# Kernel optimization log

Hardware: AMD Instinct MI355X
Metric: run time of the kernel (lower is better)

Reference implementation:

```python
import jax, jax.numpy as jnp
import numpy as np

B, S, D = 2, 1024, 4096
H, KVH = 32, 8
HD = D // H          # 128
N_REP = H // KVH     # 4
R = 2                # LoRA rank


def setup_inputs() -> dict:
    key = jax.random.key(0)
    ks = jax.random.split(key, 10)
    sc = 0.02
    x = jax.random.normal(ks[0], (B, S, D), jnp.float32)
    wq = jax.random.normal(ks[1], (D, H * HD), jnp.float32) * sc
    wk = jax.random.normal(ks[2], (D, KVH * HD), jnp.float32) * sc
    wv = jax.random.normal(ks[3], (D, KVH * HD), jnp.float32) * sc
    wo = jax.random.normal(ks[4], (H * HD, D), jnp.float32) * sc
    lora_q_a = jax.random.normal(ks[5], (D, R), jnp.float32) * sc
    lora_q_b = jax.random.normal(ks[6], (R, H * HD), jnp.float32) * sc
    lora_v_a = jax.random.normal(ks[7], (D, R), jnp.float32) * sc
    lora_v_b = jax.random.normal(ks[8], (R, KVH * HD), jnp.float32) * sc
    # RoPE frequencies: freqs_cis[t, i] = exp(1j * t * 10000^(-2i/HD))
    inv_freq = 1.0 / (10000.0 ** (jnp.arange(0, HD, 2, dtype=jnp.float32) / HD))  # [HD/2]
    t = jnp.arange(S, dtype=jnp.float32)
    ang = jnp.outer(t, inv_freq)                      # [S, HD/2]
    freqs_cos = jnp.cos(ang)
    freqs_sin = jnp.sin(ang)
    # causal additive mask [1, 1, S, S]
    mask = jnp.triu(jnp.full((S, S), -1e9, jnp.float32), k=1)[None, None]
    return {"x": x, "wq": wq, "wk": wk, "wv": wv, "wo": wo,
            "lora_q_a": lora_q_a, "lora_q_b": lora_q_b,
            "lora_v_a": lora_v_a, "lora_v_b": lora_v_b,
            "freqs_cos": freqs_cos, "freqs_sin": freqs_sin,
            "mask": mask, "start_pos": 0}


def _rope(t, cos, sin):
    # t: [B, S, h, HD]; pairs (even, odd) are (real, imag) of complex halves
    b, s, h, hd = t.shape
    tr = t.reshape(b, s, h, hd // 2, 2)
    a, bb = tr[..., 0], tr[..., 1]
    c = cos[None, :, None, :]
    sn = sin[None, :, None, :]
    out = jnp.stack([a * c - bb * sn, a * sn + bb * c], axis=-1)
    return out.reshape(b, s, h, hd)


def reference(x, wq, wk, wv, wo, lora_q_a, lora_q_b, lora_v_a, lora_v_b,
              freqs_cos, freqs_sin, mask, start_pos):
    # projections + LoRA (note: original Lora_layer applies NO scaling in forward)
    xq = x @ wq + (x @ lora_q_a) @ lora_q_b            # [B,S,H*HD]
    xk = x @ wk                                         # [B,S,KVH*HD]
    xv = x @ wv + (x @ lora_v_a) @ lora_v_b             # [B,S,KVH*HD]
    xq = xq.reshape(B, S, H, HD)
    xk = xk.reshape(B, S, KVH, HD)
    xv = xv.reshape(B, S, KVH, HD)
    xq = _rope(xq, freqs_cos, freqs_sin)
    xk = _rope(xk, freqs_cos, freqs_sin)
    # repeat_kv (GQA expansion): [B,S,KVH,HD] -> [B,S,H,HD]
    k = jnp.repeat(xk, N_REP, axis=2)
    v = jnp.repeat(xv, N_REP, axis=2)
    # attention
    scores = jnp.einsum('bshd,bthd->bhst', xq, k) / np.sqrt(HD).astype(np.float32)
    scores = scores + mask
    probs = jax.nn.softmax(scores.astype(jnp.float32), axis=-1).astype(xq.dtype)
    out = jnp.einsum('bhst,bthd->bshd', probs, v)       # [B,S,H,HD]
    out = out.reshape(B, S, H * HD) @ wo                # [B,S,D]
    return out
```

## Files before the change

kernel.cpp:

```cpp
#include <hip/hip_runtime.h>
#include <stdint.h>

#define B_ 2
#define S_ 1024
#define D_ 4096
#define H_ 32
#define KVH_ 8
#define HD_ 128

typedef short short8 __attribute__((ext_vector_type(8)));
typedef float floatx4 __attribute__((ext_vector_type(4)));

__device__ __forceinline__ ushort f2bf(float f) {
  union { float f; uint32_t u; } v; v.f = f;
  return (ushort)((v.u + 0x7FFFu + ((v.u >> 16) & 1u)) >> 16);
}

__device__ __forceinline__ void gload16(const void* g, void* l) {
  __builtin_amdgcn_global_load_lds((__attribute__((address_space(1))) void*)g,
                                   (__attribute__((address_space(3))) void*)l,
                                   16, 0, 0);
}

__global__ __launch_bounds__(256) void k_cvtlora(const float* __restrict__ x,
                                                 const float* __restrict__ qa,
                                                 const float* __restrict__ va,
                                                 ushort* __restrict__ xb,
                                                 float* __restrict__ xa) {
  const int row = blockIdx.x, t = threadIdx.x;
  const float* xr = x + (size_t)row * D_;
  ushort* xo = xb + (size_t)row * D_;
  float a0 = 0, a1 = 0, a2 = 0, a3 = 0;
#pragma unroll
  for (int it = 0; it < 4; it++) {
    const int i = it * 1024 + t * 4;
    float4 v = *(const float4*)(xr + i);
    ushort o4[4] = {f2bf(v.x), f2bf(v.y), f2bf(v.z), f2bf(v.w)};
    *(uint2*)(xo + i) = *(uint2*)o4;
    float4 q0 = *(const float4*)(qa + 2 * i);
    float4 q1 = *(const float4*)(qa + 2 * i + 4);
    float4 w0 = *(const float4*)(va + 2 * i);
    float4 w1 = *(const float4*)(va + 2 * i + 4);
    a0 += v.x * q0.x + v.y * q0.z + v.z * q1.x + v.w * q1.z;
    a1 += v.x * q0.y + v.y * q0.w + v.z * q1.y + v.w * q1.w;
    a2 += v.x * w0.x + v.y * w0.z + v.z * w1.x + v.w * w1.z;
    a3 += v.x * w0.y + v.y * w0.w + v.z * w1.y + v.w * w1.w;
  }
#pragma unroll
  for (int off = 32; off; off >>= 1) {
    a0 += __shfl_down(a0, off, 64);
    a1 += __shfl_down(a1, off, 64);
    a2 += __shfl_down(a2, off, 64);
    a3 += __shfl_down(a3, off, 64);
  }
  __shared__ float red[4][4];
  const int w = t >> 6, lane = t & 63;
  if (lane == 0) { red[w][0] = a0; red[w][1] = a1; red[w][2] = a2; red[w][3] = a3; }
  __syncthreads();
  if (t < 4)
    xa[(size_t)row * 4 + t] = red[0][t] + red[1][t] + red[2][t] + red[3][t];
}

__global__ __launch_bounds__(256) void k_tr4(const float* __restrict__ in,
                                             ushort* __restrict__ out,
                                             int in_stride, int out_stride) {
  __shared__ float t[64][65];
  const int n0 = blockIdx.x * 64, k0 = blockIdx.y * 64;
  const int c4 = (threadIdx.x & 15) * 4, r = threadIdx.x >> 4;
#pragma unroll
  for (int rr = 0; rr < 64; rr += 16) {
    float4 v = *(const float4*)&in[(size_t)(k0 + r + rr) * in_stride + n0 + c4];
    t[r + rr][c4] = v.x; t[r + rr][c4 + 1] = v.y;
    t[r + rr][c4 + 2] = v.z; t[r + rr][c4 + 3] = v.w;
  }
  __syncthreads();
#pragma unroll
  for (int rr = 0; rr < 64; rr += 16) {
    const int n = r + rr;
    ushort o4[4] = {f2bf(t[c4][n]), f2bf(t[c4 + 1][n]),
                    f2bf(t[c4 + 2][n]), f2bf(t[c4 + 3][n])};
    *(uint2*)&out[(size_t)(n0 + n) * out_stride + k0 + c4] = *(uint2*)o4;
  }
}

__global__ __launch_bounds__(256) void k_add(const float* __restrict__ a,
                                             const float* __restrict__ b,
                                             float* __restrict__ o, int n4) {
  int i = blockIdx.x * 256 + threadIdx.x;
  if (i >= n4) return;
  float4 x = ((const float4*)a)[i], y = ((const float4*)b)[i];
  float4 r = {x.x + y.x, x.y + y.y, x.z + y.z, x.w + y.w};
  ((float4*)o)[i] = r;
}

#define GBAR __builtin_amdgcn_s_barrier()
#define LGKM0 asm volatile("s_waitcnt lgkmcnt(0)" ::: "memory")
#define LGKM8 asm volatile("s_waitcnt lgkmcnt(8)" ::: "memory")
#define VMCNT0 asm volatile("s_waitcnt vmcnt(0)" ::: "memory")

#define QSTAGE_A(KT) do {                                                    \
    const ushort* gp_ = A + (size_t)(m0 + w * 16 + srow) * Kz + (KT) * 64 + scol; \
    char* lp_ = qlds + ((KT) & 1) * 65536 + w * 2048;                        \
    gload16(gp_, lp_);  gload16(gp_ + 8 * Kz, lp_ + 1024);                   \
  } while (0)

#define QSTAGE_B(U, KT) do {                                                 \
    const ushort* gp_ = Bt + (size_t)(n0 + (U) * 128 + w * 16 + srow) * Kz   \
                          + (KT) * 64 + scol;                                \
    char* lp_ = qlds + ((KT) & 1) * 65536 + 16384 + (U) * 16384 + w * 2048;  \
    gload16(gp_, lp_);  gload16(gp_ + 8 * Kz, lp_ + 1024);                   \
  } while (0)

#define QLOAD_AF(BUF) do {                                                   \
    const char* ab_ = qlds + (BUF) * 65536 + (wr * 64 + lr) * 128;           \
    _Pragma("unroll") for (int fr = 0; fr < 4; fr++)                         \
    _Pragma("unroll") for (int ks = 0; ks < 2; ks++)                         \
      af[fr][ks] = *(const short8*)(ab_ + fr * 2048 + (((ks * 4 + g) * 16) ^ swz)); \
  } while (0)

#define QLOAD_BF(J, BUF) do {                                                \
    const char* bb_ = qlds + (BUF) * 65536 + 16384 + (J) * 16384 + (wc * 32 + lr) * 128; \
    _Pragma("unroll") for (int e = 0; e < 2; e++)                            \
    _Pragma("unroll") for (int ks = 0; ks < 2; ks++)                         \
      bf[e][ks] = *(const short8*)(bb_ + e * 2048 + (((ks * 4 + g) * 16) ^ swz)); \
  } while (0)

#define QMFMA(J) do {                                                        \
    __builtin_amdgcn_s_setprio(1);                                           \
    _Pragma("unroll") for (int fr = 0; fr < 4; fr++)                         \
    _Pragma("unroll") for (int e = 0; e < 2; e++)                            \
    _Pragma("unroll") for (int ks = 0; ks < 2; ks++)                         \
      acc[fr][(J) * 2 + e] = __builtin_amdgcn_mfma_f32_16x16x32_bf16(        \
          af[fr][ks], bf[e][ks], acc[fr][(J) * 2 + e], 0, 0, 0);             \
    __builtin_amdgcn_s_setprio(0);                                           \
  } while (0)

__global__ __launch_bounds__(512, 2) void k_gemmq(const ushort* __restrict__ A,
                                                  const ushort* __restrict__ Bt,
                                                  float* __restrict__ C,
                                                  const float* __restrict__ xa,
                                                  const float* __restrict__ qb,
                                                  const float* __restrict__ vb) {
  __shared__ char qlds[131072];
  const int flat = blockIdx.y * 16 + blockIdx.x;
  const int swz_id = (flat & 7) * 32 + (flat >> 3);
  const int m0 = (swz_id >> 4) * 128, n0 = (swz_id & 15) * 384;
  const int tid = threadIdx.x, lane = tid & 63, w = tid >> 6;
  const int wr = w >> 2, wc = w & 3;
  const int lr = lane & 15, g = lane >> 4;
  const int swz = (lr & 7) * 16;
  const size_t Kz = 4096;
  const int NK = 64;
  const int srow = lane >> 3;
  const int scol = ((lane & 7) ^ (srow & 7)) * 8;

  floatx4 acc[4][6] = {};
  short8 af[4][2], bf[2][2];

  QSTAGE_A(0); QSTAGE_B(0, 0); QSTAGE_B(1, 0); QSTAGE_B(2, 0);
  QSTAGE_A(1); QSTAGE_B(0, 1); QSTAGE_B(1, 1);
  asm volatile("s_waitcnt vmcnt(10)" ::: "memory");
  GBAR;

  for (int t = 0; t < NK; ++t) {
    const int c = t & 1;
    QLOAD_AF(c); QLOAD_BF(0, c);
    if (t + 1 < NK) QSTAGE_B(2, t + 1);
    LGKM8;
    GBAR; LGKM0; QMFMA(0);
    if (t >= NK - 1) { VMCNT0; }
    else { asm volatile("s_waitcnt vmcnt(10)" ::: "memory"); }
    GBAR;
    QLOAD_BF(1, c);
    if (t + 2 < NK) { QSTAGE_A(t + 2); QSTAGE_B(0, t + 2); }
    GBAR; LGKM0; QMFMA(1);
    if (t >= NK - 2) { VMCNT0; }
    else { asm volatile("s_waitcnt vmcnt(12)" ::: "memory"); }
    GBAR;
    QLOAD_BF(2, c);
    if (t + 2 < NK) QSTAGE_B(1, t + 2);
    GBAR; LGKM0; QMFMA(2);
    if (t >= NK - 2) { VMCNT0; }
    else { asm volatile("s_waitcnt vmcnt(10)" ::: "memory"); }
    GBAR;
  }

#pragma unroll
  for (int fr = 0; fr < 4; fr++) {
    const int mb = m0 + wr * 64 + fr * 16 + g * 4;
    float4 xa4[4];
#pragma unroll
    for (int r = 0; r < 4; r++) xa4[r] = *(const float4*)&xa[(size_t)(mb + r) * 4];
#pragma unroll
    for (int j = 0; j < 3; j++)
#pragma unroll
      for (int e = 0; e < 2; e++) {
        const int n = n0 + j * 128 + wc * 32 + e * 16 + lr;
        const bool lq = (n < 4096), lv = (n >= 5120);
        float b0 = 0.f, b1 = 0.f;
        if (lq) { b0 = qb[n]; b1 = qb[4096 + n]; }
        else if (lv) { b0 = vb[n - 5120]; b1 = vb[1024 + n - 5120]; }
#pragma unroll
        for (int r = 0; r < 4; r++) {
          float cc = acc[fr][j * 2 + e][r];
          if (lq)      cc += xa4[r].x * b0 + xa4[r].y * b1;
          else if (lv) cc += xa4[r].z * b0 + xa4[r].w * b1;
          C[(size_t)(mb + r) * 6144 + n] = cc;
        }
      }
  }
}

#define STAGE_A(HALF, KT) do {                                               \
    const ushort* gp_ = A + (size_t)(m0 + (HALF) * 128 + w * 16 + srow) * Kz \
                          + kz0 + (KT) * 64 + scol;                          \
    char* lp_ = lds + ((KT) & 1) * 65536 + (HALF) * 16384 + w * 2048;        \
    gload16(gp_, lp_);                                                       \
    gload16(gp_ + 8 * Kz, lp_ + 1024);                                       \
  } while (0)

#define STAGE_B(HALF, KT) do {                                               \
    const ushort* gp_ = Bt + (size_t)(n0 + (HALF) * 128 + w * 16 + srow) * Kz\
                          + kz0 + (KT) * 64 + scol;                          \
    char* lp_ = lds + ((KT) & 1) * 65536 + 32768 + (HALF) * 16384 + w * 2048;\
    gload16(gp_, lp_);                                                       \
    gload16(gp_ + 8 * Kz, lp_ + 1024);                                       \
  } while (0)

#define LOAD_AF(QA, BUF) do {                                                \
    const char* ab_ = lds + (BUF) * 65536 + (QA) * 16384 + (wr * 64 + lr) * 128; \
    _Pragma("unroll") for (int fr = 0; fr < 4; fr++)                         \
    _Pragma("unroll") for (int ks = 0; ks < 2; ks++)                         \
      af[fr][ks] = *(const short8*)(ab_ + fr * 2048 + (((ks * 4 + g) * 16) ^ swz)); \
  } while (0)

#define LOAD_BF(QB, BUF, BF) do {                                            \
    const char* bb_ = lds + (BUF) * 65536 + 32768 + (QB) * 16384 + (wc * 32 + lr) * 128; \
    _Pragma("unroll") for (int fc = 0; fc < 2; fc++)                         \
    _Pragma("unroll") for (int ks = 0; ks < 2; ks++)                         \
      BF[fc][ks] = *(const short8*)(bb_ + fc * 2048 + (((ks * 4 + g) * 16) ^ swz)); \
  } while (0)

#define MFMA16(QA, QB, BF) do {                                              \
    __builtin_amdgcn_s_setprio(1);                                           \
    _Pragma("unroll") for (int fr = 0; fr < 4; fr++)                         \
    _Pragma("unroll") for (int fc = 0; fc < 2; fc++)                         \
    _Pragma("unroll") for (int ks = 0; ks < 2; ks++)                         \
      acc[(QA) * 4 + fr][(QB) * 2 + fc] = __builtin_amdgcn_mfma_f32_16x16x32_bf16( \
          af[fr][ks], BF[fc][ks], acc[(QA) * 4 + fr][(QB) * 2 + fc], 0, 0, 0);     \
    __builtin_amdgcn_s_setprio(0);                                           \
  } while (0)

#define VMCNT6 asm volatile("s_waitcnt vmcnt(6)" ::: "memory")

__global__ __launch_bounds__(512, 2) void k_gemm8(const ushort* __restrict__ A,
                                                  const ushort* __restrict__ Bt,
                                                  float* __restrict__ C0,
                                                  float* __restrict__ C1,
                                                  int N, int K) {
  __shared__ char lds[131072];
  const int nbx = gridDim.x;
  const int nwg = nbx * gridDim.y;
  const int flat = blockIdx.y * nbx + blockIdx.x;
  const int swz_id = (flat & 7) * (nwg >> 3) + (flat >> 3);
  const int m0 = (swz_id / nbx) * 256, n0 = (swz_id % nbx) * 256;
  const int kspan = K / gridDim.z;
  const int kz0 = blockIdx.z * kspan;
  const int NK = kspan >> 6;
  const int NJ = NK >> 1;
  float* __restrict__ Cout = blockIdx.z ? C1 : C0;

  const int tid = threadIdx.x, lane = tid & 63, w = tid >> 6;
  const int wr = w >> 2, wc = w & 3;
  const int lr = lane & 15, g = lane >> 4;
  const int swz = (lr & 7) * 16;
  const size_t Kz = (size_t)K;
  const int srow = lane >> 3;
  const int scol = ((lane & 7) ^ (srow & 7)) * 8;

  floatx4 acc[8][4] = {};
  short8 af[4][2], bf0[2][2], bf1[2][2];

  STAGE_A(0, 0); STAGE_B(0, 0); STAGE_A(1, 0); STAGE_B(1, 0);
  STAGE_A(0, 1); STAGE_B(0, 1); STAGE_A(1, 1);
  VMCNT6;
  GBAR;

  for (int j = 0; j < NJ; ++j) {
    const int t0 = 2 * j, t1 = 2 * j + 1;
    const bool last = (j == NJ - 1);
    LOAD_AF(0, 0);
    LOAD_BF(0, 0, bf0);
    STAGE_B(1, t1);
    GBAR; LGKM0; MFMA16(0, 0, bf0); GBAR;
    LOAD_BF(1, 0, bf1);
    if (t0 + 2 < NK) STAGE_A(0, t0 + 2);
    GBAR; LGKM0; MFMA16(0, 1, bf1); GBAR;
    LOAD_AF(1, 0);
    if (t0 + 2 < NK) STAGE_B(0, t0 + 2);
    GBAR; LGKM0; MFMA16(1, 1, bf1); GBAR;
    if (t0 + 2 < NK) STAGE_A(1, t0 + 2);
    if (last) { VMCNT0; } else { VMCNT6; }
    GBAR; LGKM0; MFMA16(1, 0, bf0); GBAR;
    LOAD_AF(0, 1);
    LOAD_BF(0, 1, bf0);
    if (t0 + 2 < NK) STAGE_B(1, t0 + 2);
    GBAR; LGKM0; MFMA16(0, 0, bf0); GBAR;
    LOAD_BF(1, 1, bf1);
    if (t1 + 2 < NK) STAGE_A(0, t1 + 2);
    GBAR; LGKM0; MFMA16(0, 1, bf1); GBAR;
    LOAD_AF(1, 1);
    if (t1 + 2 < NK) STAGE_B(0, t1 + 2);
    GBAR; LGKM0; MFMA16(1, 1, bf1); GBAR;
    if (t1 + 2 < NK) STAGE_A(1, t1 + 2);
    if (last) { VMCNT0; } else { VMCNT6; }
    GBAR; LGKM0; MFMA16(1, 0, bf0); GBAR;
  }

#pragma unroll
  for (int qa = 0; qa < 2; qa++)
#pragma unroll
    for (int fr = 0; fr < 4; fr++) {
      const int mb = m0 + qa * 128 + wr * 64 + fr * 16 + g * 4;
#pragma unroll
      for (int qb_ = 0; qb_ < 2; qb_++)
#pragma unroll
        for (int fc = 0; fc < 2; fc++) {
          const int n = n0 + qb_ * 128 + wc * 32 + fc * 16 + lr;
#pragma unroll
          for (int r = 0; r < 4; r++)
            Cout[(size_t)(mb + r) * N + n] = acc[qa * 4 + fr][qb_ * 2 + fc][r];
        }
    }
}

__global__ __launch_bounds__(256) void k_rope(const float* __restrict__ xqkv,
                                              const float* __restrict__ fcos,
                                              const float* __restrict__ fsin,
                                              ushort* __restrict__ Qb,
                                              ushort* __restrict__ Kb) {
  const int s = blockIdx.x, b = blockIdx.y;
  const float* row = xqkv + (size_t)(b * S_ + s) * 6144;
#pragma unroll
  for (int it = 0; it < 8; it++) {
    int p2 = it * 256 + threadIdx.x;
    int h = p2 >> 6, p = p2 & 63;
    float2 ab = *(const float2*)(row + h * 128 + 2 * p);
    float c = fcos[s * 64 + p], sn = fsin[s * 64 + p];
    uint32_t pk = (uint32_t)f2bf(ab.x * c - ab.y * sn) |
                  ((uint32_t)f2bf(ab.x * sn + ab.y * c) << 16);
    *(uint32_t*)(Qb + ((size_t)(b * H_ + h) * S_ + s) * HD_ + 2 * p) = pk;
  }
#pragma unroll
  for (int it = 0; it < 2; it++) {
    int p2 = it * 256 + threadIdx.x;
    int h = p2 >> 6, p = p2 & 63;
    float2 ab = *(const float2*)(row + 4096 + h * 128 + 2 * p);
    float c = fcos[s * 64 + p], sn = fsin[s * 64 + p];
    uint32_t pk = (uint32_t)f2bf(ab.x * c - ab.y * sn) |
                  ((uint32_t)f2bf(ab.x * sn + ab.y * c) << 16);
    *(uint32_t*)(Kb + ((size_t)(b * KVH_ + h) * S_ + s) * HD_ + 2 * p) = pk;
  }
}

#define FSTAGE(T, DB) do {                                                   \
    _Pragma("unroll") for (int i_ = 0; i_ < 4; i_++) {                       \
      gload16(Kg + (size_t)((T) * 64 + i_ * 16 + k_srow) * HD_ + k_scol,     \
              fls + (DB) * 16384 + i_ * 4096 + w * 1024);                    \
      gload16(Vg + (size_t)(i_ * 32 + v_srow) * S_ + (T) * 64 + v_scol,      \
              fls + 32768 + (DB) * 16384 + i_ * 4096 + w * 1024);            \
    }                                                                        \
  } while (0)

__global__ __launch_bounds__(256, 2) void k_flash(const ushort* __restrict__ Qb,
                                                  const ushort* __restrict__ Kb,
                                                  const ushort* __restrict__ Vt,
                                                  ushort* __restrict__ attn) {
  __shared__ char fls[73728];
  const int qblk = (gridDim.x - 1) - blockIdx.x;
  const int h = blockIdx.y, b = blockIdx.z;
  const int kvh = h >> 2;
  const int tid = threadIdx.x, w = tid >> 6, lane = tid & 63;
  const int lr = lane & 15, g = lane >> 4;
  const int swz = (lr & 7) * 16;
  const int qr0 = qblk * 64 + w * 16;
  const ushort* Qrow = Qb + ((size_t)(b * H_ + h) * S_ + qr0 + lr) * HD_;
  short8 qf[4];
#pragma unroll
  for (int ks = 0; ks < 4; ks++) qf[ks] = *(const short8*)(Qrow + ks * 32 + g * 8);
  const ushort* Kg = Kb + (size_t)(b * KVH_ + kvh) * S_ * HD_;
  const ushort* Vg = Vt + (size_t)(b * KVH_ + kvh) * HD_ * S_;
  char* Pw = fls + 65536 + w * 2048;
  const int q7 = lr & 7;
  const int k_srow = tid >> 4;
  const int k_scol = ((tid & 15) ^ (k_srow & 7)) * 8;
  const int v_srow = tid >> 3;
  const int v_scol = ((tid & 7) ^ (v_srow & 7)) * 8;

  float m_run = -1e30f, l_run = 0.f;
  floatx4 o[8] = {};
  const int nt = qblk + 1;

  FSTAGE(0, 0);
  asm volatile("s_waitcnt vmcnt(0)" ::: "memory");
  __builtin_amdgcn_s_barrier();

  for (int t = 0; t < nt; t++) {
    const int cur = t & 1;
    if (t + 1 < nt) FSTAGE(t + 1, cur ^ 1);
    const char* Kl = fls + cur * 16384;
    const char* Vl = fls + 32768 + cur * 16384;
    floatx4 s4[4] = {};
    __builtin_amdgcn_s_setprio(1);
#pragma unroll
    for (int mf = 0; mf < 4; mf++) {
      const char* Krow = Kl + (mf * 16 + lr) * 256;
#pragma unroll
      for (int ks = 0; ks < 4; ks++) {
        short8 kf = *(const short8*)(Krow + (((ks * 4 + g) * 16) ^ swz));
        s4[mf] = __builtin_amdgcn_mfma_f32_16x16x32_bf16(kf, qf[ks], s4[mf], 0, 0, 0);
      }
    }
    __builtin_amdgcn_s_setprio(0);
    const float scale = 0.088388347648318447f;
    float tm = -1e30f;
    if (t == nt - 1) {
#pragma unroll
      for (int mf = 0; mf < 4; mf++)
#pragma unroll
        for (int r = 0; r < 4; r++) {
          int kv = t * 64 + mf * 16 + g * 4 + r;
          float v = (kv > qr0 + lr) ? -1e30f : s4[mf][r] * scale;
          s4[mf][r] = v;
          tm = fmaxf(tm, v);
        }
    } else {
#pragma unroll
      for (int mf = 0; mf < 4; mf++)
#pragma unroll
        for (int r = 0; r < 4; r++) {
          float v = s4[mf][r] * scale;
          s4[mf][r] = v;
          tm = fmaxf(tm, v);
        }
    }
    tm = fmaxf(tm, __shfl_xor(tm, 16, 64));
    tm = fmaxf(tm, __shfl_xor(tm, 32, 64));
    float m_new = fmaxf(m_run, tm);
    float corr = __expf(m_run - m_new);
    float rs = 0.f;
#pragma unroll
    for (int mf = 0; mf < 4; mf++)
#pragma unroll
      for (int r = 0; r < 4; r++) {
        float p = __expf(s4[mf][r] - m_new);
        s4[mf][r] = p;
        rs += p;
      }
    rs += __shfl_xor(rs, 16, 64);
    rs += __shfl_xor(rs, 32, 64);
    l_run = l_run * corr + rs;
    m_run = m_new;
#pragma unroll
    for (int r = 0; r < 4; r++) {
      float cr = __shfl(corr, g * 4 + r, 64);
#pragma unroll
      for (int nf = 0; nf < 8; nf++) o[nf][r] *= cr;
    }
#pragma unroll
    for (int mf = 0; mf < 4; mf++) {
      uint2 pv;
      pv.x = (uint32_t)f2bf(s4[mf][0]) | ((uint32_t)f2bf(s4[mf][1]) << 16);
      pv.y = (uint32_t)f2bf(s4[mf][2]) | ((uint32_t)f2bf(s4[mf][3]) << 16);
      *(uint2*)(Pw + lr * 128 + ((mf * 32 + g * 8) ^ (q7 << 4))) = pv;
    }
    __builtin_amdgcn_s_setprio(1);
#pragma unroll
    for (int ks2 = 0; ks2 < 2; ks2++) {
      short8 pa = *(const short8*)(Pw + lr * 128 + ((ks2 * 64 + g * 16) ^ (q7 << 4)));
#pragma unroll
      for (int nf = 0; nf < 8; nf++) {
        short8 vf = *(const short8*)(Vl + (nf * 16 + lr) * 128 + (((ks2 * 4 + g) * 16) ^ swz));
        o[nf] = __builtin_amdgcn_mfma_f32_16x16x32_bf16(pa, vf, o[nf], 0, 0, 0);
      }
    }
    __builtin_amdgcn_s_setprio(0);
    asm volatile("s_waitcnt vmcnt(0)" ::: "memory");
    __builtin_amdgcn_s_barrier();
  }
  float linv = 1.0f / l_run;
  ushort* outp = attn + ((size_t)(b * S_) + qr0) * 4096 + h * 128;
#pragma unroll
  for (int r = 0; r < 4; r++) {
    float li = __shfl(linv, g * 4 + r, 64);
    ushort* orow = outp + (size_t)(g * 4 + r) * 4096;
#pragma unroll
    for (int nf = 0; nf < 8; nf++)
      orow[nf * 16 + lr] = f2bf(o[nf][r] * li);
  }
}

extern "C" void kernel_launch(void* const* d_in, const int* in_sizes, int n_in,
                              void* d_out, int out_size, void* d_ws, size_t ws_size,
                              hipStream_t stream) {
  (void)in_sizes; (void)n_in; (void)out_size; (void)ws_size;
  const float* x    = (const float*)d_in[0];
  const float* wq   = (const float*)d_in[1];
  const float* wk   = (const float*)d_in[2];
  const float* wv   = (const float*)d_in[3];
  const float* wo   = (const float*)d_in[4];
  const float* lqa  = (const float*)d_in[5];
  const float* lqb  = (const float*)d_in[6];
  const float* lva  = (const float*)d_in[7];
  const float* lvb  = (const float*)d_in[8];
  const float* fcos = (const float*)d_in[9];
  const float* fsin = (const float*)d_in[10];

  char* ws = (char*)d_ws;
  ushort* xb   = (ushort*)(ws + 0);
  ushort* wT   = (ushort*)(ws + 16777216);
  ushort* woT  = (ushort*)(ws + 67108864);
  float*  xqkv = (float*) (ws + 100663296);
  ushort* Qb   = (ushort*)(ws + 150994944);
  ushort* Kb   = (ushort*)(ws + 167772160);
  ushort* Vt   = (ushort*)(ws + 171966464);
  ushort* attn = (ushort*)(ws + 176160768);
  float*  xa   = (float*) (ws + 192937984);
  float*  p0   = (float*) (ws + 16777216);
  float*  p1   = (float*) (ws + 100663296);

  k_cvtlora<<<2048, 256, 0, stream>>>(x, lqa, lva, xb, xa);
  k_tr4<<<dim3(64, 64), 256, 0, stream>>>(wq, wT, 4096, 4096);
  k_tr4<<<dim3(16, 64), 256, 0, stream>>>(wk, wT + (size_t)4096 * 4096, 1024, 4096);
  k_tr4<<<dim3(16, 64), 256, 0, stream>>>(wv, wT + (size_t)5120 * 4096, 1024, 4096);
  k_tr4<<<dim3(64, 64), 256, 0, stream>>>(wo, woT, 4096, 4096);
  k_gemmq<<<dim3(16, 16), 512, 0, stream>>>(xb, wT, xqkv, xa, lqb, lvb);
  k_rope<<<dim3(1024, 2), 256, 0, stream>>>(xqkv, fcos, fsin, Qb, Kb);
  k_tr4<<<dim3(16, 16), 256, 0, stream>>>(xqkv + 5120, Vt, 6144, 1024);
  k_tr4<<<dim3(16, 16), 256, 0, stream>>>(xqkv + (size_t)1024 * 6144 + 5120, Vt + 1048576, 6144, 1024);
  k_flash<<<dim3(16, 32, 2), 256, 0, stream>>>(Qb, Kb, Vt, attn);
  k_gemm8<<<dim3(16, 8, 2), 512, 0, stream>>>(attn, woT, p0, p1, 4096, 4096);
  k_add<<<8192, 256, 0, stream>>>(p0, p1, (float*)d_out, 2097152);
}
```

Baseline: 335.1 us.

## Fuse launches, emit bf16 QKV with transposed V, widen flash tiles, drop split-K

Merges the weight-transpose launches into two z-indexed kernels. The QKV GEMM now writes bf16 Q/K and transposed V directly, which removes the fp32 intermediate and the separate V transpose kernels. The flash kernel processes 128 query rows per block with two accumulators that share K/V tiles, halving K/V traffic per query. The output projection replaces split-K plus an add kernel with a single 128x256-tile GEMM writing the output directly. The trade-offs are fewer blocks in flash and the output GEMM, lower occupancy potential, and bf16 rounding of the projections before RoPE.

```diff
diff --git a/kernel.cpp b/kernel.cpp
--- a/kernel.cpp
+++ b/kernel.cpp
@@ -14,6 +14,9 @@
 __device__ __forceinline__ ushort f2bf(float f) {
   union { float f; uint32_t u; } v; v.f = f;
   return (ushort)((v.u + 0x7FFFu + ((v.u >> 16) & 1u)) >> 16);
+}
+__device__ __forceinline__ float bf2f(ushort u) {
+  union { uint32_t x; float f; } v; v.x = ((uint32_t)u) << 16; return v.f;
 }
 
 __device__ __forceinline__ void gload16(const void* g, void* l) {
@@ -61,9 +64,13 @@
     xa[(size_t)row * 4 + t] = red[0][t] + red[1][t] + red[2][t] + red[3][t];
 }
 
-__global__ __launch_bounds__(256) void k_tr4(const float* __restrict__ in,
-                                             ushort* __restrict__ out,
-                                             int in_stride, int out_stride) {
+__global__ __launch_bounds__(256) void k_trw2(const float* __restrict__ in0,
+                                              const float* __restrict__ in1,
+                                              ushort* __restrict__ out0,
+                                              ushort* __restrict__ out1,
+                                              int in_stride, int out_stride) {
+  const float* in = blockIdx.z ? in1 : in0;
+  ushort* out = blockIdx.z ? out1 : out0;
   __shared__ float t[64][65];
   const int n0 = blockIdx.x * 64, k0 = blockIdx.y * 64;
   const int c4 = (threadIdx.x & 15) * 4, r = threadIdx.x >> 4;
@@ -83,20 +90,12 @@
   }
 }
 
-__global__ __launch_bounds__(256) void k_add(const float* __restrict__ a,
-                                             const float* __restrict__ b,
-                                             float* __restrict__ o, int n4) {
-  int i = blockIdx.x * 256 + threadIdx.x;
-  if (i >= n4) return;
-  float4 x = ((const float4*)a)[i], y = ((const float4*)b)[i];
-  float4 r = {x.x + y.x, x.y + y.y, x.z + y.z, x.w + y.w};
-  ((float4*)o)[i] = r;
-}
-
 #define GBAR __builtin_amdgcn_s_barrier()
 #define LGKM0 asm volatile("s_waitcnt lgkmcnt(0)" ::: "memory")
 #define LGKM8 asm volatile("s_waitcnt lgkmcnt(8)" ::: "memory")
 #define VMCNT0 asm volatile("s_waitcnt vmcnt(0)" ::: "memory")
+#define VMCNT2 asm volatile("s_waitcnt vmcnt(2)" ::: "memory")
+#define VMCNT6 asm volatile("s_waitcnt vmcnt(6)" ::: "memory")
 
 #define QSTAGE_A(KT) do {                                                    \
     const ushort* gp_ = A + (size_t)(m0 + w * 16 + srow) * Kz + (KT) * 64 + scol; \
@@ -137,7 +136,8 @@
 
 __global__ __launch_bounds__(512, 2) void k_gemmq(const ushort* __restrict__ A,
                                                   const ushort* __restrict__ Bt,
-                                                  float* __restrict__ C,
+                                                  ushort* __restrict__ xq,
+                                                  ushort* __restrict__ Vt,
                                                   const float* __restrict__ xa,
                                                   const float* __restrict__ qb,
                                                   const float* __restrict__ vb) {
@@ -188,6 +188,7 @@
 #pragma unroll
   for (int fr = 0; fr < 4; fr++) {
     const int mb = m0 + wr * 64 + fr * 16 + g * 4;
+    const int bb = mb >> 10, s0 = mb & 1023;
     float4 xa4[4];
 #pragma unroll
     for (int r = 0; r < 4; r++) xa4[r] = *(const float4*)&xa[(size_t)(mb + r) * 4];
@@ -196,169 +197,149 @@
 #pragma unroll
       for (int e = 0; e < 2; e++) {
         const int n = n0 + j * 128 + wc * 32 + e * 16 + lr;
-        const bool lq = (n < 4096), lv = (n >= 5120);
-        float b0 = 0.f, b1 = 0.f;
-        if (lq) { b0 = qb[n]; b1 = qb[4096 + n]; }
-        else if (lv) { b0 = vb[n - 5120]; b1 = vb[1024 + n - 5120]; }
-#pragma unroll
-        for (int r = 0; r < 4; r++) {
-          float cc = acc[fr][j * 2 + e][r];
-          if (lq)      cc += xa4[r].x * b0 + xa4[r].y * b1;
-          else if (lv) cc += xa4[r].z * b0 + xa4[r].w * b1;
-          C[(size_t)(mb + r) * 6144 + n] = cc;
+        if (n < 5120) {
+          const bool lq = (n < 4096);
+          float b0 = 0.f, b1 = 0.f;
+          if (lq) { b0 = qb[n]; b1 = qb[4096 + n]; }
+#pragma unroll
+          for (int r = 0; r < 4; r++) {
+            float cc = acc[fr][j * 2 + e][r];
+            if (lq) cc += xa4[r].x * b0 + xa4[r].y * b1;
+            xq[(size_t)(mb + r) * 6144 + n] = f2bf(cc);
+          }
+        } else {
+          const int vcol = n - 5120;
+          const float b0 = vb[vcol], b1 = vb[1024 + vcol];
+          ushort v4[4];
+#pragma unroll
+          for (int r = 0; r < 4; r++)
+            v4[r] = f2bf(acc[fr][j * 2 + e][r] + xa4[r].z * b0 + xa4[r].w * b1);
+          *(uint2*)&Vt[(size_t)((bb * 8 + (vcol >> 7)) * 128 + (vcol & 127)) * 1024 + s0] =
+              *(uint2*)v4;
         }
       }
   }
 }
 
-#define STAGE_A(HALF, KT) do {                                               \
-    const ushort* gp_ = A + (size_t)(m0 + (HALF) * 128 + w * 16 + srow) * Kz \
-                          + kz0 + (KT) * 64 + scol;                          \
-    char* lp_ = lds + ((KT) & 1) * 65536 + (HALF) * 16384 + w * 2048;        \
-    gload16(gp_, lp_);                                                       \
-    gload16(gp_ + 8 * Kz, lp_ + 1024);                                       \
-  } while (0)
-
-#define STAGE_B(HALF, KT) do {                                               \
-    const ushort* gp_ = Bt + (size_t)(n0 + (HALF) * 128 + w * 16 + srow) * Kz\
-                          + kz0 + (KT) * 64 + scol;                          \
-    char* lp_ = lds + ((KT) & 1) * 65536 + 32768 + (HALF) * 16384 + w * 2048;\
-    gload16(gp_, lp_);                                                       \
-    gload16(gp_ + 8 * Kz, lp_ + 1024);                                       \
-  } while (0)
-
-#define LOAD_AF(QA, BUF) do {                                                \
-    const char* ab_ = lds + (BUF) * 65536 + (QA) * 16384 + (wr * 64 + lr) * 128; \
+#define OSTAGE_A(KT) do {                                                    \
+    const ushort* gp_ = A + (size_t)(m0 + w * 16 + srow) * Kz + (KT) * 64 + scol; \
+    char* lp_ = olds + ((KT) & 1) * 49152 + w * 2048;                        \
+    gload16(gp_, lp_);  gload16(gp_ + 8 * Kz, lp_ + 1024);                   \
+  } while (0)
+
+#define OSTAGE_B(U, KT) do {                                                 \
+    const ushort* gp_ = Bt + (size_t)(n0 + (U) * 128 + w * 16 + srow) * Kz   \
+                          + (KT) * 64 + scol;                                \
+    char* lp_ = olds + ((KT) & 1) * 49152 + 16384 + (U) * 16384 + w * 2048;  \
+    gload16(gp_, lp_);  gload16(gp_ + 8 * Kz, lp_ + 1024);                   \
+  } while (0)
+
+#define OLOAD_AF(BUF) do {                                                   \
+    const char* ab_ = olds + (BUF) * 49152 + (wr * 64 + lr) * 128;           \
     _Pragma("unroll") for (int fr = 0; fr < 4; fr++)                         \
     _Pragma("unroll") for (int ks = 0; ks < 2; ks++)                         \
       af[fr][ks] = *(const short8*)(ab_ + fr * 2048 + (((ks * 4 + g) * 16) ^ swz)); \
   } while (0)
 
-#define LOAD_BF(QB, BUF, BF) do {                                            \
-    const char* bb_ = lds + (BUF) * 65536 + 32768 + (QB) * 16384 + (wc * 32 + lr) * 128; \
-    _Pragma("unroll") for (int fc = 0; fc < 2; fc++)                         \
+#define OLOAD_BF(U, BUF) do {                                                \
+    const char* bb_ = olds + (BUF) * 49152 + 16384 + (U) * 16384 + (wc * 32 + lr) * 128; \
+    _Pragma("unroll") for (int e = 0; e < 2; e++)                            \
     _Pragma("unroll") for (int ks = 0; ks < 2; ks++)                         \
-      BF[fc][ks] = *(const short8*)(bb_ + fc * 2048 + (((ks * 4 + g) * 16) ^ swz)); \
-  } while (0)
-
-#define MFMA16(QA, QB, BF) do {                                              \
+      bf[e][ks] = *(const short8*)(bb_ + e * 2048 + (((ks * 4 + g) * 16) ^ swz)); \
+  } while (0)
+
+#define OMFMA(U) do {                                                        \
     __builtin_amdgcn_s_setprio(1);                                           \
     _Pragma("unroll") for (int fr = 0; fr < 4; fr++)                         \
-    _Pragma("unroll") for (int fc = 0; fc < 2; fc++)                         \
+    _Pragma("unroll") for (int e = 0; e < 2; e++)                            \
     _Pragma("unroll") for (int ks = 0; ks < 2; ks++)                         \
-      acc[(QA) * 4 + fr][(QB) * 2 + fc] = __builtin_amdgcn_mfma_f32_16x16x32_bf16( \
-          af[fr][ks], BF[fc][ks], acc[(QA) * 4 + fr][(QB) * 2 + fc], 0, 0, 0);     \
+      acc[fr][(U) * 2 + e] = __builtin_amdgcn_mfma_f32_16x16x32_bf16(        \
+          af[fr][ks], bf[e][ks], acc[fr][(U) * 2 + e], 0, 0, 0);             \
     __builtin_amdgcn_s_setprio(0);                                           \
   } while (0)
 
-#define VMCNT6 asm volatile("s_waitcnt vmcnt(6)" ::: "memory")
-
-__global__ __launch_bounds__(512, 2) void k_gemm8(const ushort* __restrict__ A,
+__global__ __launch_bounds__(512, 2) void k_gemmo(const ushort* __restrict__ A,
                                                   const ushort* __restrict__ Bt,
-                                                  float* __restrict__ C0,
-                                                  float* __restrict__ C1,
-                                                  int N, int K) {
-  __shared__ char lds[131072];
-  const int nbx = gridDim.x;
-  const int nwg = nbx * gridDim.y;
-  const int flat = blockIdx.y * nbx + blockIdx.x;
-  const int swz_id = (flat & 7) * (nwg >> 3) + (flat >> 3);
-  const int m0 = (swz_id / nbx) * 256, n0 = (swz_id % nbx) * 256;
-  const int kspan = K / gridDim.z;
-  const int kz0 = blockIdx.z * kspan;
-  const int NK = kspan >> 6;
-  const int NJ = NK >> 1;
-  float* __restrict__ Cout = blockIdx.z ? C1 : C0;
-
+                                                  float* __restrict__ C) {
+  __shared__ char olds[98304];
+  const int flat = blockIdx.y * 16 + blockIdx.x;
+  const int swz_id = (flat & 7) * 32 + (flat >> 3);
+  const int m0 = (swz_id >> 4) * 128, n0 = (swz_id & 15) * 256;
   const int tid = threadIdx.x, lane = tid & 63, w = tid >> 6;
   const int wr = w >> 2, wc = w & 3;
   const int lr = lane & 15, g = lane >> 4;
   const int swz = (lr & 7) * 16;
-  const size_t Kz = (size_t)K;
+  const size_t Kz = 4096;
+  const int NK = 64;
   const int srow = lane >> 3;
   const int scol = ((lane & 7) ^ (srow & 7)) * 8;
 
-  floatx4 acc[8][4] = {};
-  short8 af[4][2], bf0[2][2], bf1[2][2];
-
-  STAGE_A(0, 0); STAGE_B(0, 0); STAGE_A(1, 0); STAGE_B(1, 0);
-  STAGE_A(0, 1); STAGE_B(0, 1); STAGE_A(1, 1);
-  VMCNT6;
+  floatx4 acc[4][4] = {};
+  short8 af[4][2], bf[2][2];
+
+  OSTAGE_A(0); OSTAGE_B(0, 0); OSTAGE_B(1, 0);
+  OSTAGE_A(1); OSTAGE_B(0, 1);
+  asm volatile("s_waitcnt vmcnt(4)" ::: "memory");
   GBAR;
 
-  for (int j = 0; j < NJ; ++j) {
-    const int t0 = 2 * j, t1 = 2 * j + 1;
-    const bool last = (j == NJ - 1);
-    LOAD_AF(0, 0);
-    LOAD_BF(0, 0, bf0);
-    STAGE_B(1, t1);
-    GBAR; LGKM0; MFMA16(0, 0, bf0); GBAR;
-    LOAD_BF(1, 0, bf1);
-    if (t0 + 2 < NK) STAGE_A(0, t0 + 2);
-    GBAR; LGKM0; MFMA16(0, 1, bf1); GBAR;
-    LOAD_AF(1, 0);
-    if (t0 + 2 < NK) STAGE_B(0, t0 + 2);
-    GBAR; LGKM0; MFMA16(1, 1, bf1); GBAR;
-    if (t0 + 2 < NK) STAGE_A(1, t0 + 2);
-    if (last) { VMCNT0; } else { VMCNT6; }
-    GBAR; LGKM0; MFMA16(1, 0, bf0); GBAR;
-    LOAD_AF(0, 1);
-    LOAD_BF(0, 1, bf0);
-    if (t0 + 2 < NK) STAGE_B(1, t0 + 2);
-    GBAR; LGKM0; MFMA16(0, 0, bf0); GBAR;
-    LOAD_BF(1, 1, bf1);
-    if (t1 + 2 < NK) STAGE_A(0, t1 + 2);
-    GBAR; LGKM0; MFMA16(0, 1, bf1); GBAR;
-    LOAD_AF(1, 1);
-    if (t1 + 2 < NK) STAGE_B(0, t1 + 2);
-    GBAR; LGKM0; MFMA16(1, 1, bf1); GBAR;
-    if (t1 + 2 < NK) STAGE_A(1, t1 + 2);
-    if (last) { VMCNT0; } else { VMCNT6; }
-    GBAR; LGKM0; MFMA16(1, 0, bf0); GBAR;
-  }
-
-#pragma unroll
-  for (int qa = 0; qa < 2; qa++)
-#pragma unroll
-    for (int fr = 0; fr < 4; fr++) {
-      const int mb = m0 + qa * 128 + wr * 64 + fr * 16 + g * 4;
-#pragma unroll
-      for (int qb_ = 0; qb_ < 2; qb_++)
-#pragma unroll
-        for (int fc = 0; fc < 2; fc++) {
-          const int n = n0 + qb_ * 128 + wc * 32 + fc * 16 + lr;
-#pragma unroll
-          for (int r = 0; r < 4; r++)
-            Cout[(size_t)(mb + r) * N + n] = acc[qa * 4 + fr][qb_ * 2 + fc][r];
-        }
-    }
-}
-
-__global__ __launch_bounds__(256) void k_rope(const float* __restrict__ xqkv,
+  for (int t = 0; t < NK; ++t) {
+    const int c = t & 1;
+    OLOAD_AF(c); OLOAD_BF(0, c);
+    if (t + 1 < NK) OSTAGE_B(1, t + 1);
+    LGKM8;
+    GBAR; LGKM0; OMFMA(0);
+    if (t == NK - 1) { VMCNT0; } else { VMCNT6; }
+    GBAR;
+    OLOAD_BF(1, c);
+    if (t + 2 < NK) { OSTAGE_A(t + 2); OSTAGE_B(0, t + 2); }
+    GBAR; LGKM0; OMFMA(1);
+    if (t < NK - 2) { VMCNT6; }
+    else if (t == NK - 2) { VMCNT2; }
+    GBAR;
+  }
+
+#pragma unroll
+  for (int fr = 0; fr < 4; fr++) {
+    const int mb = m0 + wr * 64 + fr * 16 + g * 4;
+#pragma unroll
+    for (int j = 0; j < 2; j++)
+#pragma unroll
+      for (int e = 0; e < 2; e++) {
+        const int n = n0 + j * 128 + wc * 32 + e * 16 + lr;
+#pragma unroll
+        for (int r = 0; r < 4; r++)
+          C[(size_t)(mb + r) * 4096 + n] = acc[fr][j * 2 + e][r];
+      }
+  }
+}
+
+__global__ __launch_bounds__(256) void k_rope(const ushort* __restrict__ xq,
                                               const float* __restrict__ fcos,
                                               const float* __restrict__ fsin,
                                               ushort* __restrict__ Qb,
                                               ushort* __restrict__ Kb) {
   const int s = blockIdx.x, b = blockIdx.y;
-  const float* row = xqkv + (size_t)(b * S_ + s) * 6144;
+  const ushort* row = xq + (size_t)(b * S_ + s) * 6144;
 #pragma unroll
   for (int it = 0; it < 8; it++) {
     int p2 = it * 256 + threadIdx.x;
     int h = p2 >> 6, p = p2 & 63;
-    float2 ab = *(const float2*)(row + h * 128 + 2 * p);
+    uint32_t u = *(const uint32_t*)(row + h * 128 + 2 * p);
+    float a = bf2f((ushort)u), bb = bf2f((ushort)(u >> 16));
     float c = fcos[s * 64 + p], sn = fsin[s * 64 + p];
-    uint32_t pk = (uint32_t)f2bf(ab.x * c - ab.y * sn) |
-                  ((uint32_t)f2bf(ab.x * sn + ab.y * c) << 16);
+    uint32_t pk = (uint32_t)f2bf(a * c - bb * sn) |
+                  ((uint32_t)f2bf(a * sn + bb * c) << 16);
     *(uint32_t*)(Qb + ((size_t)(b * H_ + h) * S_ + s) * HD_ + 2 * p) = pk;
   }
 #pragma unroll
   for (int it = 0; it < 2; it++) {
     int p2 = it * 256 + threadIdx.x;
     int h = p2 >> 6, p = p2 & 63;
-    float2 ab = *(const float2*)(row + 4096 + h * 128 + 2 * p);
+    uint32_t u = *(const uint32_t*)(row + 4096 + h * 128 + 2 * p);
+    float a = bf2f((ushort)u), bb = bf2f((ushort)(u >> 16));
     float c = fcos[s * 64 + p], sn = fsin[s * 64 + p];
-    uint32_t pk = (uint32_t)f2bf(ab.x * c - ab.y * sn) |
-                  ((uint32_t)f2bf(ab.x * sn + ab.y * c) << 16);
+    uint32_t pk = (uint32_t)f2bf(a * c - bb * sn) |
+                  ((uint32_t)f2bf(a * sn + bb * c) << 16);
     *(uint32_t*)(Kb + ((size_t)(b * KVH_ + h) * S_ + s) * HD_ + 2 * p) = pk;
   }
 }
@@ -376,127 +357,198 @@
                                                   const ushort* __restrict__ Kb,
                                                   const ushort* __restrict__ Vt,
                                                   ushort* __restrict__ attn) {
-  __shared__ char fls[73728];
+  __shared__ char fls[81920];
   const int qblk = (gridDim.x - 1) - blockIdx.x;
   const int h = blockIdx.y, b = blockIdx.z;
   const int kvh = h >> 2;
   const int tid = threadIdx.x, w = tid >> 6, lane = tid & 63;
   const int lr = lane & 15, g = lane >> 4;
   const int swz = (lr & 7) * 16;
-  const int qr0 = qblk * 64 + w * 16;
-  const ushort* Qrow = Qb + ((size_t)(b * H_ + h) * S_ + qr0 + lr) * HD_;
-  short8 qf[4];
-#pragma unroll
-  for (int ks = 0; ks < 4; ks++) qf[ks] = *(const short8*)(Qrow + ks * 32 + g * 8);
+  const int qra = qblk * 128 + w * 16;
+  const ushort* Qrow = Qb + ((size_t)(b * H_ + h) * S_ + qra + lr) * HD_;
+  short8 qfa[4], qfb[4];
+#pragma unroll
+  for (int ks = 0; ks < 4; ks++) {
+    qfa[ks] = *(const short8*)(Qrow + ks * 32 + g * 8);
+    qfb[ks] = *(const short8*)(Qrow + 64 * HD_ + ks * 32 + g * 8);
+  }
   const ushort* Kg = Kb + (size_t)(b * KVH_ + kvh) * S_ * HD_;
   const ushort* Vg = Vt + (size_t)(b * KVH_ + kvh) * HD_ * S_;
-  char* Pw = fls + 65536 + w * 2048;
+  char* Pw = fls + 65536 + w * 4096;
   const int q7 = lr & 7;
   const int k_srow = tid >> 4;
   const int k_scol = ((tid & 15) ^ (k_srow & 7)) * 8;
   const int v_srow = tid >> 3;
   const int v_scol = ((tid & 7) ^ (v_srow & 7)) * 8;
-
-  float m_run = -1e30f, l_run = 0.f;
-  floatx4 o[8] = {};
-  const int nt = qblk + 1;
+  const float scale = 0.088388347648318447f;
+
+  float m_a = -1e30f, l_a = 0.f, m_b = -1e30f, l_b = 0.f;
+  floatx4 oa[8] = {}, ob[8] = {};
+  const int nt = 2 * qblk + 2;
+  const int lastA = 2 * qblk;
 
   FSTAGE(0, 0);
-  asm volatile("s_waitcnt vmcnt(0)" ::: "memory");
-  __builtin_amdgcn_s_barrier();
+  VMCNT0;
+  GBAR;
 
   for (int t = 0; t < nt; t++) {
     const int cur = t & 1;
     if (t + 1 < nt) FSTAGE(t + 1, cur ^ 1);
     const char* Kl = fls + cur * 16384;
     const char* Vl = fls + 32768 + cur * 16384;
-    floatx4 s4[4] = {};
+    if (t <= lastA) {
+      floatx4 s4[4] = {};
+      __builtin_amdgcn_s_setprio(1);
+#pragma unroll
+      for (int mf = 0; mf < 4; mf++) {
+        const char* Krow = Kl + (mf * 16 + lr) * 256;
+#pragma unroll
+        for (int ks = 0; ks < 4; ks++) {
+          short8 kf = *(const short8*)(Krow + (((ks * 4 + g) * 16) ^ swz));
+          s4[mf] = __builtin_amdgcn_mfma_f32_16x16x32_bf16(kf, qfa[ks], s4[mf], 0, 0, 0);
+        }
+      }
+      __builtin_amdgcn_s_setprio(0);
+      float tm = -1e30f;
+      if (t == lastA) {
+#pragma unroll
+        for (int mf = 0; mf < 4; mf++)
+#pragma unroll
+          for (int r = 0; r < 4; r++) {
+            int kv = t * 64 + mf * 16 + g * 4 + r;
+            float v = (kv > qra + lr) ? -1e30f : s4[mf][r] * scale;
+            s4[mf][r] = v; tm = fmaxf(tm, v);
+          }
+      } else {
+#pragma unroll
+        for (int mf = 0; mf < 4; mf++)
+#pragma unroll
+          for (int r = 0; r < 4; r++) {
+            float v = s4[mf][r] * scale;
+            s4[mf][r] = v; tm = fmaxf(tm, v);
+          }
+      }
+      tm = fmaxf(tm, __shfl_xor(tm, 16, 64));
+      tm = fmaxf(tm, __shfl_xor(tm, 32, 64));
+      float m_new = fmaxf(m_a, tm);
+      float corr = __expf(m_a - m_new);
+      float rs = 0.f;
+#pragma unroll
+      for (int mf = 0; mf < 4; mf++)
+#pragma unroll
+        for (int r = 0; r < 4; r++) {
+          float p = __expf(s4[mf][r] - m_new);
+          s4[mf][r] = p; rs += p;
+        }
+      rs += __shfl_xor(rs, 16, 64);
+      rs += __shfl_xor(rs, 32, 64);
+      l_a = l_a * corr + rs; m_a = m_new;
+#pragma unroll
+      for (int r = 0; r < 4; r++) {
+        float cr = __shfl(corr, g * 4 + r, 64);
+#pragma unroll
+        for (int nf = 0; nf < 8; nf++) oa[nf][r] *= cr;
+      }
+#pragma unroll
+      for (int mf = 0; mf < 4; mf++) {
+        uint2 pv;
+        pv.x = (uint32_t)f2bf(s4[mf][0]) | ((uint32_t)f2bf(s4[mf][1]) << 16);
+        pv.y = (uint32_t)f2bf(s4[mf][2]) | ((uint32_t)f2bf(s4[mf][3]) << 16);
+        *(uint2*)(Pw + lr * 128 + ((mf * 32 + g * 8) ^ (q7 << 4))) = pv;
+      }
+    }
+    {
+      floatx4 s4[4] = {};
+      __builtin_amdgcn_s_setprio(1);
+#pragma unroll
+      for (int mf = 0; mf < 4; mf++) {
+        const char* Krow = Kl + (mf * 16 + lr) * 256;
+#pragma unroll
+        for (int ks = 0; ks < 4; ks++) {
+          short8 kf = *(const short8*)(Krow + (((ks * 4 + g) * 16) ^ swz));
+          s4[mf] = __builtin_amdgcn_mfma_f32_16x16x32_bf16(kf, qfb[ks], s4[mf], 0, 0, 0);
+        }
+      }
+      __builtin_amdgcn_s_setprio(0);
+      float tm = -1e30f;
+      if (t == nt - 1) {
+#pragma unroll
+        for (int mf = 0; mf < 4; mf++)
+#pragma unroll
+          for (int r = 0; r < 4; r++) {
+            int kv = t * 64 + mf * 16 + g * 4 + r;
+            float v = (kv > qra + 64 + lr) ? -1e30f : s4[mf][r] * scale;
+            s4[mf][r] = v; tm = fmaxf(tm, v);
+          }
+      } else {
+#pragma unroll
+        for (int mf = 0; mf < 4; mf++)
+#pragma unroll
+          for (int r = 0; r < 4; r++) {
+            float v = s4[mf][r] * scale;
+            s4[mf][r] = v; tm = fmaxf(tm, v);
+          }
+      }
+      tm = fmaxf(tm, __shfl_xor(tm, 16, 64));
+      tm = fmaxf(tm, __shfl_xor(tm, 32, 64));
+      float m_new = fmaxf(m_b, tm);
+      float corr = __expf(m_b - m_new);
+      float rs = 0.f;
+#pragma unroll
+      for (int mf = 0; mf < 4; mf++)
+#pragma unroll
+        for (int r = 0; r < 4; r++) {
+          float p = __expf(s4[mf][r] - m_new);
+          s4[mf][r] = p; rs += p;
+        }
+      rs += __shfl_xor(rs, 16, 64);
+      rs += __shfl_xor(rs, 32, 64);
+      l_b = l_b * corr + rs; m_b = m_new;
+#pragma unroll
+      for (int r = 0; r < 4; r++) {
+        float cr = __shfl(corr, g * 4 + r, 64);
+#pragma unroll
+        for (int nf = 0; nf < 8; nf++) ob[nf][r] *= cr;
+      }
+#pragma unroll
+      for (int mf = 0; mf < 4; mf++) {
+        uint2 pv;
+        pv.x = (uint32_t)f2bf(s4[mf][0]) | ((uint32_t)f2bf(s4[mf][1]) << 16);
+        pv.y = (uint32_t)f2bf(s4[mf][2]) | ((uint32_t)f2bf(s4[mf][3]) << 16);
+        *(uint2*)(Pw + 2048 + lr * 128 + ((mf * 32 + g * 8) ^ (q7 << 4))) = pv;
+      }
+    }
     __builtin_amdgcn_s_setprio(1);
 #pragma unroll
-    for (int mf = 0; mf < 4; mf++) {
-      const char* Krow = Kl + (mf * 16 + lr) * 256;
-#pragma unroll
-      for (int ks = 0; ks < 4; ks++) {
-        short8 kf = *(const short8*)(Krow + (((ks * 4 + g) * 16) ^ swz));
-        s4[mf] = __builtin_amdgcn_mfma_f32_16x16x32_bf16(kf, qf[ks], s4[mf], 0, 0, 0);
+    for (int ks2 = 0; ks2 < 2; ks2++) {
+      short8 pb = *(const short8*)(Pw + 2048 + lr * 128 + ((ks2 * 64 + g * 16) ^ (q7 << 4)));
+      short8 pa = pb;
+      if (t <= lastA)
+        pa = *(const short8*)(Pw + lr * 128 + ((ks2 * 64 + g * 16) ^ (q7 << 4)));
+#pragma unroll
+      for (int nf = 0; nf < 8; nf++) {
+        short8 vf = *(const short8*)(Vl + (nf * 16 + lr) * 128 + (((ks2 * 4 + g) * 16) ^ swz));
+        if (t <= lastA)
+          oa[nf] = __builtin_amdgcn_mfma_f32_16x16x32_bf16(pa, vf, oa[nf], 0, 0, 0);
+        ob[nf] = __builtin_amdgcn_mfma_f32_16x16x32_bf16(pb, vf, ob[nf], 0, 0, 0);
       }
     }
     __builtin_amdgcn_s_setprio(0);
-    const float scale = 0.088388347648318447f;
-    float tm = -1e30f;
-    if (t == nt - 1) {
-#pragma unroll
-      for (int mf = 0; mf < 4; mf++)
-#pragma unroll
-        for (int r = 0; r < 4; r++) {
-          int kv = t * 64 + mf * 16 + g * 4 + r;
-          float v = (kv > qr0 + lr) ? -1e30f : s4[mf][r] * scale;
-          s4[mf][r] = v;
-          tm = fmaxf(tm, v);
-        }
-    } else {
-#pragma unroll
-      for (int mf = 0; mf < 4; mf++)
-#pragma unroll
-        for (int r = 0; r < 4; r++) {
-          float v = s4[mf][r] * scale;
-          s4[mf][r] = v;
-          tm = fmaxf(tm, v);
-        }
+    VMCNT0;
+    GBAR;
+  }
+  const float linva = 1.0f / l_a, linvb = 1.0f / l_b;
+  ushort* outp = attn + ((size_t)(b * S_) + qra) * 4096 + h * 128;
+#pragma unroll
+  for (int r = 0; r < 4; r++) {
+    float lia = __shfl(linva, g * 4 + r, 64);
+    float lib = __shfl(linvb, g * 4 + r, 64);
+    ushort* orow = outp + (size_t)(g * 4 + r) * 4096;
+#pragma unroll
+    for (int nf = 0; nf < 8; nf++) {
+      orow[nf * 16 + lr] = f2bf(oa[nf][r] * lia);
+      orow[(size_t)64 * 4096 + nf * 16 + lr] = f2bf(ob[nf][r] * lib);
     }
-    tm = fmaxf(tm, __shfl_xor(tm, 16, 64));
-    tm = fmaxf(tm, __shfl_xor(tm, 32, 64));
-    float m_new = fmaxf(m_run, tm);
-    float corr = __expf(m_run - m_new);
-    float rs = 0.f;
-#pragma unroll
-    for (int mf = 0; mf < 4; mf++)
-#pragma unroll
-      for (int r = 0; r < 4; r++) {
-        float p = __expf(s4[mf][r] - m_new);
-        s4[mf][r] = p;
-        rs += p;
-      }
-    rs += __shfl_xor(rs, 16, 64);
-    rs += __shfl_xor(rs, 32, 64);
-    l_run = l_run * corr + rs;
-    m_run = m_new;
-#pragma unroll
-    for (int r = 0; r < 4; r++) {
-      float cr = __shfl(corr, g * 4 + r, 64);
-#pragma unroll
-      for (int nf = 0; nf < 8; nf++) o[nf][r] *= cr;
-    }
-#pragma unroll
-    for (int mf = 0; mf < 4; mf++) {
-      uint2 pv;
-      pv.x = (uint32_t)f2bf(s4[mf][0]) | ((uint32_t)f2bf(s4[mf][1]) << 16);
-      pv.y = (uint32_t)f2bf(s4[mf][2]) | ((uint32_t)f2bf(s4[mf][3]) << 16);
-      *(uint2*)(Pw + lr * 128 + ((mf * 32 + g * 8) ^ (q7 << 4))) = pv;
-    }
-    __builtin_amdgcn_s_setprio(1);
-#pragma unroll
-    for (int ks2 = 0; ks2 < 2; ks2++) {
-      short8 pa = *(const short8*)(Pw + lr * 128 + ((ks2 * 64 + g * 16) ^ (q7 << 4)));
-#pragma unroll
-      for (int nf = 0; nf < 8; nf++) {
-        short8 vf = *(const short8*)(Vl + (nf * 16 + lr) * 128 + (((ks2 * 4 + g) * 16) ^ swz));
-        o[nf] = __builtin_amdgcn_mfma_f32_16x16x32_bf16(pa, vf, o[nf], 0, 0, 0);
-      }
-    }
-    __builtin_amdgcn_s_setprio(0);
-    asm volatile("s_waitcnt vmcnt(0)" ::: "memory");
-    __builtin_amdgcn_s_barrier();
-  }
-  float linv = 1.0f / l_run;
-  ushort* outp = attn + ((size_t)(b * S_) + qr0) * 4096 + h * 128;
-#pragma unroll
-  for (int r = 0; r < 4; r++) {
-    float li = __shfl(linv, g * 4 + r, 64);
-    ushort* orow = outp + (size_t)(g * 4 + r) * 4096;
-#pragma unroll
-    for (int nf = 0; nf < 8; nf++)
-      orow[nf * 16 + lr] = f2bf(o[nf][r] * li);
   }
 }
 
@@ -520,25 +572,19 @@
   ushort* xb   = (ushort*)(ws + 0);
   ushort* wT   = (ushort*)(ws + 16777216);
   ushort* woT  = (ushort*)(ws + 67108864);
-  float*  xqkv = (float*) (ws + 100663296);
+  ushort* xq   = (ushort*)(ws + 100663296);
   ushort* Qb   = (ushort*)(ws + 150994944);
   ushort* Kb   = (ushort*)(ws + 167772160);
   ushort* Vt   = (ushort*)(ws + 171966464);
   ushort* attn = (ushort*)(ws + 176160768);
   float*  xa   = (float*) (ws + 192937984);
-  float*  p0   = (float*) (ws + 16777216);
-  float*  p1   = (float*) (ws + 100663296);
 
   k_cvtlora<<<2048, 256, 0, stream>>>(x, lqa, lva, xb, xa);
-  k_tr4<<<dim3(64, 64), 256, 0, stream>>>(wq, wT, 4096, 4096);
-  k_tr4<<<dim3(16, 64), 256, 0, stream>>>(wk, wT + (size_t)4096 * 4096, 1024, 4096);
-  k_tr4<<<dim3(16, 64), 256, 0, stream>>>(wv, wT + (size_t)5120 * 4096, 1024, 4096);
-  k_tr4<<<dim3(64, 64), 256, 0, stream>>>(wo, woT, 4096, 4096);
-  k_gemmq<<<dim3(16, 16), 512, 0, stream>>>(xb, wT, xqkv, xa, lqb, lvb);
-  k_rope<<<dim3(1024, 2), 256, 0, stream>>>(xqkv, fcos, fsin, Qb, Kb);
-  k_tr4<<<dim3(16, 16), 256, 0, stream>>>(xqkv + 5120, Vt, 6144, 1024);
-  k_tr4<<<dim3(16, 16), 256, 0, stream>>>(xqkv + (size_t)1024 * 6144 + 5120, Vt + 1048576, 6144, 1024);
-  k_flash<<<dim3(16, 32, 2), 256, 0, stream>>>(Qb, Kb, Vt, attn);
-  k_gemm8<<<dim3(16, 8, 2), 512, 0, stream>>>(attn, woT, p0, p1, 4096, 4096);
-  k_add<<<8192, 256, 0, stream>>>(p0, p1, (float*)d_out, 2097152);
-}
+  k_trw2<<<dim3(64, 64, 2), 256, 0, stream>>>(wq, wo, wT, woT, 4096, 4096);
+  k_trw2<<<dim3(16, 64, 2), 256, 0, stream>>>(wk, wv, wT + (size_t)4096 * 4096,
+                                              wT + (size_t)5120 * 4096, 1024, 4096);
+  k_gemmq<<<dim3(16, 16), 512, 0, stream>>>(xb, wT, xq, Vt, xa, lqb, lvb);
+  k_rope<<<dim3(1024, 2), 256, 0, stream>>>(xq, fcos, fsin, Qb, Kb);
+  k_flash<<<dim3(8, 32, 2), 256, 0, stream>>>(Qb, Kb, Vt, attn);
+  k_gemmo<<<dim3(16, 16), 512, 0, stream>>>(attn, woT, (float*)d_out);
+}
```

After: 301.9 us. -9.9%, faster.
